# Optimization experiments

Hardware: AMD Instinct MI355X
Metric: run time of the kernel (lower is better)

## Reference

```python
import jax, jax.numpy as jnp
import numpy as np

WS = 8            # current window
PRETRAIN = 8      # pretrain window
HEADS = 8
C = 256
UNITS = C // HEADS
SHIFT = WS // 2   # shift_mode=1 -> shift_dir=[1,1], apply_shift True (H,W > WS)
EPS = 1.55e-5
LOG100 = float(np.log(100.0))

# ---- static relative-position index and log-spaced coord table (SwinV2 CPB) ----
_c = np.arange(WS)
_rel_h = _c[:, None] - _c[None, :] + (WS - 1)          # [WS,WS] in [0, 2WS-2]
REL_INDEX = (_rel_h[:, None, :, None] * (2 * WS - 1) + _rel_h[None, :, None, :]).reshape(WS * WS, WS * WS)
_r = np.arange(-(WS - 1), WS, dtype=np.float32)
_t = np.stack(np.meshgrid(_r, _r, indexing='ij'), axis=-1).reshape(-1, 2)  # [(2WS-1)^2, 2]
_t = _t / (PRETRAIN - 1) * 8.0
CPB_TABLE = np.sign(_t) * np.log2(1.0 + np.abs(_t)) / np.log2(8.0)


def _shift_mask(H, W):
    # region labels per Swin shift mask: segments (dim-WS, WS-SHIFT, SHIFT) for shift_dir=+1
    def seg(n):
        s = np.zeros(n, np.int32)
        s[n - WS:n - SHIFT] = 1
        s[n - SHIFT:] = 2
        return s
    img = seg(H)[:, None] * 3 + seg(W)[None, :] + 1      # [H,W]
    img = img.reshape(H // WS, WS, W // WS, WS).transpose(0, 2, 1, 3).reshape(-1, WS * WS)
    d = img[:, :, None] - img[:, None, :]
    return np.where(d == 0, 0.0, -100.0).astype(np.float32)  # [nW, WS^2, WS^2]

SHIFT_MASK = _shift_mask(256, 256)


def _partition(t, H, W):
    # [B,H,W,C] -> [B,nW,heads,WS^2,units]
    B = t.shape[0]
    t = t.reshape(B, H // WS, WS, W // WS, WS, HEADS, UNITS)
    t = t.transpose(0, 1, 3, 5, 2, 4, 6)
    return t.reshape(B, (H // WS) * (W // WS), HEADS, WS * WS, UNITS)


def _reverse(t, H, W):
    B = t.shape[0]
    t = t.reshape(B, H // WS, W // WS, HEADS, WS, WS, UNITS)
    t = t.transpose(0, 1, 4, 2, 5, 3, 6)
    return t.reshape(B, H, W, C)


def _l2n(t):
    return t / jnp.sqrt(jnp.maximum(jnp.sum(t * t, axis=-1, keepdims=True), EPS))


def setup_inputs():
    key = jax.random.key(0)
    ks = jax.random.split(key, 6)
    return {
        'x': jax.random.normal(ks[0], (2, 256, 256, C), jnp.float32),
        'qkv_w': jax.random.normal(ks[1], (C, 3 * C), jnp.float32) * 0.02,
        'q_bias': jnp.zeros((C,), jnp.float32),
        'v_bias': jnp.zeros((C,), jnp.float32),
        'scale': jnp.full((HEADS, 1, 1), np.log(10.0), jnp.float32),
        'cpb_w1': jax.random.normal(ks[2], (2, 512), jnp.float32) * 0.02,
        'cpb_b1': jnp.zeros((512,), jnp.float32),
        'cpb_w2': jax.random.normal(ks[3], (512, HEADS), jnp.float32) * 0.02,
        'proj_w': jax.random.normal(ks[4], (C, C), jnp.float32) * 0.02,
        'proj_b': jnp.zeros((C,), jnp.float32),
    }


def reference(x, qkv_w, q_bias, v_bias, scale, cpb_w1, cpb_b1, cpb_w2, proj_w, proj_b):
    B, H, W, _ = x.shape
    qkv = x @ qkv_w + jnp.concatenate([q_bias, jnp.zeros_like(q_bias), v_bias])
    qkv = jnp.roll(qkv, (-SHIFT, -SHIFT), axis=(1, 2))
    q, k, v = jnp.split(qkv, 3, axis=-1)
    q = _l2n(_partition(q, H, W))          # [B,nW,h,WS^2,u]
    k = _l2n(_partition(k, H, W))
    v = _partition(v, H, W)
    logit_scale = jnp.exp(jnp.minimum(scale, LOG100))  # [h,1,1]
    attn = jnp.einsum('bwhqd,bwhkd->bwhqk', q * logit_scale, k)
    # continuous relative position bias
    cpb = jax.nn.relu(jnp.asarray(CPB_TABLE) @ cpb_w1 + cpb_b1) @ cpb_w2  # [(2WS-1)^2, h]
    bias = 16.0 * jax.nn.sigmoid(cpb[REL_INDEX])                          # [WS^2,WS^2,h]
    bias = bias.transpose(2, 0, 1)                                        # [h,WS^2,WS^2]
    attn = attn + bias[None, None] + jnp.asarray(SHIFT_MASK)[None, :, None]
    attn = jax.nn.softmax(attn, axis=-1)
    out = jnp.einsum('bwhqk,bwhkd->bwhqd', attn, v)
    out = _reverse(out, H, W)
    out = jnp.roll(out, (SHIFT, SHIFT), axis=(1, 2))
    return out @ proj_w + proj_b
```

## Files before the change

kernel.cpp:

```cpp
#include <hip/hip_runtime.h>


typedef _Float16 f16;
typedef _Float16 f16x4 __attribute__((ext_vector_type(4)));
typedef _Float16 f16x8 __attribute__((ext_vector_type(8)));
typedef float f32x4 __attribute__((ext_vector_type(4)));

#define LOG100 4.6051701859880914f
#define EPS_L2 1.55e-5f

__device__ __forceinline__ int seg2(int p) { return (p >= 248) + (p >= 252); }

__global__ __launch_bounds__(512) void k_prep(
    const float* __restrict__ cpb_w1, const float* __restrict__ cpb_b1,
    const float* __restrict__ cpb_w2, const float* __restrict__ qkv_w,
    const float* __restrict__ proj_w,
    float* __restrict__ biasfrag, f16* __restrict__ w_t, f16* __restrict__ p_t)
{
    int tid = threadIdx.x;
    if (blockIdx.x == 0) {
        __shared__ float Lw1[1024];
        __shared__ float Lb1[512];
        __shared__ float Lw2[4096];
        __shared__ float part[450 * 8];
        __shared__ float cpb[225 * 8];
        #pragma unroll
        for (int i = tid; i < 1024; i += 512) Lw1[i] = cpb_w1[i];
        if (tid < 512) Lb1[tid] = cpb_b1[tid];
        #pragma unroll
        for (int i = tid; i < 4096; i += 512) Lw2[i] = cpb_w2[i];
        __syncthreads();
        {
            int e = tid >> 1, half = tid & 1;
            if (e < 225) {
                int a = e / 15, b2 = e % 15;
                float xa = (float)(a - 7) * (8.0f / 7.0f);
                float xb = (float)(b2 - 7) * (8.0f / 7.0f);
                float t0 = (xa < 0.f ? -1.f : 1.f) * log2f(1.0f + fabsf(xa)) * (1.0f / 3.0f);
                float t1 = (xb < 0.f ? -1.f : 1.f) * log2f(1.0f + fabsf(xb)) * (1.0f / 3.0f);
                float acc[8] = {0.f, 0.f, 0.f, 0.f, 0.f, 0.f, 0.f, 0.f};
                int j0 = half << 8;
                #pragma unroll 4
                for (int j = j0; j < j0 + 256; ++j) {
                    float hh = fmaxf(t0 * Lw1[j] + t1 * Lw1[512 + j] + Lb1[j], 0.0f);
                    #pragma unroll
                    for (int h = 0; h < 8; ++h) acc[h] += hh * Lw2[j * 8 + h];
                }
                #pragma unroll
                for (int h = 0; h < 8; ++h) part[tid * 8 + h] = acc[h];
            }
        }
        __syncthreads();
        if (tid < 225) {
            #pragma unroll
            for (int h = 0; h < 8; ++h)
                cpb[tid * 8 + h] = part[tid * 16 + h] + part[tid * 16 + 8 + h];
        }
        __syncthreads();
        for (int f = tid; f < 32768; f += 512) {
            int r = f & 3, lane = (f >> 2) & 63, nt = (f >> 8) & 3, mt = (f >> 10) & 3, h = (f >> 12) & 7;
            int k = mt * 16 + ((lane >> 4) << 2) + r;
            int q = nt * 16 + (lane & 15);
            int idx = ((q >> 3) - (k >> 3) + 7) * 15 + ((q & 7) - (k & 7) + 7);
            float c = cpb[idx * 8 + h];
            biasfrag[f] = 16.0f / (1.0f + expf(-c));
        }
    } else {
        int base = (blockIdx.x - 1) * 512 + tid;
        const int stride = 128 * 512;
        for (int i = base; i < 768 * 256; i += stride) {
            int n = i >> 8, k = i & 255;
            w_t[i] = (f16)qkv_w[k * 768 + n];
        }
        for (int i = base; i < 256 * 256; i += stride) {
            int n = i >> 8, k = i & 255;
            p_t[i] = (f16)proj_w[k * 256 + n];
        }
    }
}

__global__ __launch_bounds__(512, 3) void k_fused(
    const float* __restrict__ x, const f16* __restrict__ w_t,
    const float* __restrict__ q_bias, const float* __restrict__ v_bias,
    const float* __restrict__ scale, const float* __restrict__ biasfrag,
    const f16* __restrict__ p_t, const float* __restrict__ proj_b,
    float* __restrict__ out)
{
    __shared__ char L[65536];
    const int tid = threadIdx.x;
    const int lane = tid & 63;
    const int h = tid >> 6;
    const int l15 = lane & 15, g = lane >> 4;
    const int bw = blockIdx.x;
    const int win = bw & 1023, b = bw >> 10;
    const int wh = win >> 5, ww = win & 31;
    char* wb = L + 32768 + (h << 12);
    const f32x4 fz = {0.f, 0.f, 0.f, 0.f};
    const bool boundary = (wh == 31) || (ww == 31);

    {
        int pos = tid >> 3, tc = tid & 7;
        int i2 = ((wh << 3) + (pos >> 3) + 4) & 255;
        int j2 = ((ww << 3) + (pos & 7) + 4) & 255;
        const float* xr = x + ((((long)b << 8) + i2) * 256 + j2) * 256;
        int swz = (pos & 7) << 4;
        #pragma unroll
        for (int rep = 0; rep < 4; ++rep) {
            int ch = rep * 64 + tc * 8;
            float4 v0 = *reinterpret_cast<const float4*>(xr + ch);
            float4 v1 = *reinterpret_cast<const float4*>(xr + ch + 4);
            f16x8 hv = { (f16)v0.x, (f16)v0.y, (f16)v0.z, (f16)v0.w,
                         (f16)v1.x, (f16)v1.y, (f16)v1.z, (f16)v1.w };
            *reinterpret_cast<f16x8*>(L + ((pos * 512 + ch * 2) ^ swz)) = hv;
        }
    }
    __syncthreads();

    f16x8 qa[4], kb[4], vf[2][2];

    {
        f32x4 aqk[4][4];
        #pragma unroll
        for (int i = 0; i < 4; ++i)
            #pragma unroll
            for (int j = 0; j < 4; ++j) aqk[i][j] = fz;

        #pragma unroll
        for (int ks = 0; ks < 8; ++ks) {
            f16x8 xf[4], wqk[4];
            #pragma unroll
            for (int mt = 0; mt < 4; ++mt) {
                int row = mt * 16 + l15;
                xf[mt] = *reinterpret_cast<const f16x8*>(
                    L + ((row * 512 + ks * 64 + g * 16) ^ ((row & 7) << 4)));
            }
            #pragma unroll
            for (int ci = 0; ci < 4; ++ci) {
                int p = ci >> 1, ct = ci & 1;
                wqk[ci] = *reinterpret_cast<const f16x8*>(
                    w_t + ((p << 8) + (h << 5) + ct * 16 + l15) * 256 + ks * 32 + g * 8);
            }
            #pragma unroll
            for (int ci = 0; ci < 4; ++ci)
                #pragma unroll
                for (int mt = 0; mt < 4; ++mt)
                    aqk[ci][mt] = __builtin_amdgcn_mfma_f32_16x16x32_f16(wqk[ci], xf[mt], aqk[ci][mt], 0, 0, 0);
        }

        {
            float ls = __expf(fminf(scale[h], LOG100));
            float qb0[4], qb1[4];
            #pragma unroll
            for (int r = 0; r < 4; ++r) {
                qb0[r] = q_bias[(h << 5) + (g << 2) + r];
                qb1[r] = q_bias[(h << 5) + 16 + (g << 2) + r];
            }
            #pragma unroll
            for (int nt = 0; nt < 4; ++nt) {
                int pix = nt * 16 + l15;
                float t0[4], t1[4], s2 = 0.f;
                #pragma unroll
                for (int r = 0; r < 4; ++r) {
                    t0[r] = aqk[0][nt][r] + qb0[r];
                    t1[r] = aqk[1][nt][r] + qb1[r];
                    s2 += t0[r] * t0[r] + t1[r] * t1[r];
                }
                s2 += __shfl_xor(s2, 16); s2 += __shfl_xor(s2, 32);
                float iv = ls / sqrtf(fmaxf(s2, EPS_L2));
                int sw = (pix & 7) << 4;
                f16x4 p0 = { (f16)(t0[0] * iv), (f16)(t0[1] * iv), (f16)(t0[2] * iv), (f16)(t0[3] * iv) };
                f16x4 p1 = { (f16)(t1[0] * iv), (f16)(t1[1] * iv), (f16)(t1[2] * iv), (f16)(t1[3] * iv) };
                *reinterpret_cast<f16x4*>(wb + ((pix * 64 + (g << 3)) ^ sw)) = p0;
                *reinterpret_cast<f16x4*>(wb + ((pix * 64 + 32 + (g << 3)) ^ sw)) = p1;
            }
            #pragma unroll
            for (int nt = 0; nt < 4; ++nt)
                qa[nt] = *reinterpret_cast<const f16x8*>(
                    wb + (((nt * 16 + l15) * 64 + g * 16) ^ ((l15 & 7) << 4)));
        }
        {
            #pragma unroll
            for (int nt = 0; nt < 4; ++nt) {
                int pix = nt * 16 + l15;
                float t0[4], t1[4], s2 = 0.f;
                #pragma unroll
                for (int r = 0; r < 4; ++r) {
                    t0[r] = aqk[2][nt][r];
                    t1[r] = aqk[3][nt][r];
                    s2 += t0[r] * t0[r] + t1[r] * t1[r];
                }
                s2 += __shfl_xor(s2, 16); s2 += __shfl_xor(s2, 32);
                float iv = 1.0f / sqrtf(fmaxf(s2, EPS_L2));
                int sw = (pix & 7) << 4;
                f16x4 p0 = { (f16)(t0[0] * iv), (f16)(t0[1] * iv), (f16)(t0[2] * iv), (f16)(t0[3] * iv) };
                f16x4 p1 = { (f16)(t1[0] * iv), (f16)(t1[1] * iv), (f16)(t1[2] * iv), (f16)(t1[3] * iv) };
                *reinterpret_cast<f16x4*>(wb + ((pix * 64 + (g << 3)) ^ sw)) = p0;
                *reinterpret_cast<f16x4*>(wb + ((pix * 64 + 32 + (g << 3)) ^ sw)) = p1;
            }
            #pragma unroll
            for (int nt = 0; nt < 4; ++nt)
                kb[nt] = *reinterpret_cast<const f16x8*>(
                    wb + (((nt * 16 + l15) * 64 + g * 16) ^ ((l15 & 7) << 4)));
        }
    }

    {
        f32x4 av[4][2];
        #pragma unroll
        for (int mt = 0; mt < 4; ++mt) { av[mt][0] = fz; av[mt][1] = fz; }
        #pragma unroll
        for (int ks = 0; ks < 8; ++ks) {
            f16x8 xf[4], wv[2];
            #pragma unroll
            for (int mt = 0; mt < 4; ++mt) {
                int row = mt * 16 + l15;
                xf[mt] = *reinterpret_cast<const f16x8*>(
                    L + ((row * 512 + ks * 64 + g * 16) ^ ((row & 7) << 4)));
            }
            #pragma unroll
            for (int nt = 0; nt < 2; ++nt)
                wv[nt] = *reinterpret_cast<const f16x8*>(
                    w_t + (512 + (h << 5) + nt * 16 + l15) * 256 + ks * 32 + g * 8);
            #pragma unroll
            for (int mt = 0; mt < 4; ++mt)
                #pragma unroll
                for (int nt = 0; nt < 2; ++nt)
                    av[mt][nt] = __builtin_amdgcn_mfma_f32_16x16x32_f16(xf[mt], wv[nt], av[mt][nt], 0, 0, 0);
        }
        float b0 = v_bias[(h << 5) + l15], b1 = v_bias[(h << 5) + 16 + l15];
        #pragma unroll
        for (int mt = 0; mt < 4; ++mt)
            #pragma unroll
            for (int nt = 0; nt < 2; ++nt) {
                float bsel = nt ? b1 : b0;
                f32x4 avv = av[mt][nt];
                f16x4 pk = { (f16)(avv[0] + bsel), (f16)(avv[1] + bsel),
                             (f16)(avv[2] + bsel), (f16)(avv[3] + bsel) };
                int u = nt * 16 + l15;
                int pix0 = mt * 16 + (g << 2);
                *reinterpret_cast<f16x4*>(wb + ((u * 128 + pix0 * 2) ^ ((u & 7) << 4))) = pk;
            }
        #pragma unroll
        for (int nt = 0; nt < 2; ++nt)
            #pragma unroll
            for (int ks = 0; ks < 2; ++ks)
                vf[nt][ks] = *reinterpret_cast<const f16x8*>(
                    wb + (((nt * 16 + l15) * 128 + ks * 64 + g * 16) ^ ((l15 & 7) << 4)));
    }

    f16x4 oh[4][2];
    #pragma unroll
    for (int c = 0; c < 2; ++c) {
        #pragma unroll
        for (int n2 = 0; n2 < 2; ++n2) {
            const int nt = c * 2 + n2;
            const int qrow = nt * 16 + l15;
            f32x4 st[4];
            #pragma unroll
            for (int mt = 0; mt < 4; ++mt)
                st[mt] = __builtin_amdgcn_mfma_f32_16x16x32_f16(kb[mt], qa[nt], fz, 0, 0, 0);
            #pragma unroll
            for (int mt = 0; mt < 4; ++mt)
                st[mt] += *reinterpret_cast<const f32x4*>(
                    biasfrag + ((((h * 4 + mt) * 4 + nt) * 64 + lane) << 2));
            if (boundary) {
                int lq = seg2((wh << 3) + (qrow >> 3)) * 3 + seg2((ww << 3) + (qrow & 7));
                #pragma unroll
                for (int mt = 0; mt < 4; ++mt)
                    #pragma unroll
                    for (int r = 0; r < 4; ++r) {
                        int k = mt * 16 + (g << 2) + r;
                        int lk = seg2((wh << 3) + (k >> 3)) * 3 + seg2((ww << 3) + (k & 7));
                        if (lq != lk) st[mt][r] -= 100.0f;
                    }
            }
            float mx = st[0][0];
            #pragma unroll
            for (int mt = 0; mt < 4; ++mt)
                #pragma unroll
                for (int r = 0; r < 4; ++r) mx = fmaxf(mx, st[mt][r]);
            mx = fmaxf(mx, __shfl_xor(mx, 16));
            mx = fmaxf(mx, __shfl_xor(mx, 32));
            float sm = 0.f;
            #pragma unroll
            for (int mt = 0; mt < 4; ++mt)
                #pragma unroll
                for (int r = 0; r < 4; ++r) {
                    float e = __expf(st[mt][r] - mx);
                    st[mt][r] = e;
                    sm += e;
                }
            sm += __shfl_xor(sm, 16);
            sm += __shfl_xor(sm, 32);
            float inv = 1.0f / sm;
            int sw = (qrow & 7) << 4;
            int rowb = (qrow & 31) * 128;
            #pragma unroll
            for (int mt = 0; mt < 4; ++mt) {
                f16x4 pk = { (f16)(st[mt][0] * inv), (f16)(st[mt][1] * inv),
                             (f16)(st[mt][2] * inv), (f16)(st[mt][3] * inv) };
                *reinterpret_cast<f16x4*>(wb + ((rowb + mt * 32 + (g << 3)) ^ sw)) = pk;
            }
        }
        #pragma unroll
        for (int m2 = 0; m2 < 2; ++m2) {
            const int mt = c * 2 + m2;
            int row = m2 * 16 + l15;
            int swz = (row & 7) << 4;
            f16x8 pa0 = *reinterpret_cast<const f16x8*>(wb + ((row * 128 + g * 16) ^ swz));
            f16x8 pa1 = *reinterpret_cast<const f16x8*>(wb + ((row * 128 + 64 + g * 16) ^ swz));
            #pragma unroll
            for (int nt = 0; nt < 2; ++nt) {
                f32x4 t = __builtin_amdgcn_mfma_f32_16x16x32_f16(pa0, vf[nt][0], fz, 0, 0, 0);
                t = __builtin_amdgcn_mfma_f32_16x16x32_f16(pa1, vf[nt][1], t, 0, 0, 0);
                oh[mt][nt] = f16x4{ (f16)t[0], (f16)t[1], (f16)t[2], (f16)t[3] };
            }
        }
    }

    __syncthreads();
    #pragma unroll
    for (int mt = 0; mt < 4; ++mt)
        #pragma unroll
        for (int r = 0; r < 4; ++r) {
            int q = mt * 16 + (g << 2) + r;
            #pragma unroll
            for (int nt = 0; nt < 2; ++nt) {
                int ch = (h << 5) + nt * 16 + l15;
                *reinterpret_cast<f16*>(L + ((q * 512 + ch * 2) ^ ((q & 7) << 4))) =
                    oh[mt][nt][r];
            }
        }
    __syncthreads();

    const int c0 = h << 5;
    f32x4 pc[4][2];
    #pragma unroll
    for (int mt = 0; mt < 4; ++mt) { pc[mt][0] = fz; pc[mt][1] = fz; }
    #pragma unroll
    for (int ks = 0; ks < 8; ++ks) {
        f16x8 a[4], bfr[2];
        #pragma unroll
        for (int mt = 0; mt < 4; ++mt) {
            int q = mt * 16 + l15;
            a[mt] = *reinterpret_cast<const f16x8*>(
                L + ((q * 512 + ks * 64 + g * 16) ^ ((q & 7) << 4)));
        }
        #pragma unroll
        for (int nt = 0; nt < 2; ++nt)
            bfr[nt] = *reinterpret_cast<const f16x8*>(
                p_t + (c0 + nt * 16 + l15) * 256 + ks * 32 + g * 8);
        #pragma unroll
        for (int mt = 0; mt < 4; ++mt)
            #pragma unroll
            for (int nt = 0; nt < 2; ++nt)
                pc[mt][nt] = __builtin_amdgcn_mfma_f32_16x16x32_f16(a[mt], bfr[nt], pc[mt][nt], 0, 0, 0);
    }
    float pb0 = proj_b[c0 + l15], pb1 = proj_b[c0 + 16 + l15];
    #pragma unroll
    for (int mt = 0; mt < 4; ++mt)
        #pragma unroll
        for (int r = 0; r < 4; ++r) {
            int q = mt * 16 + (g << 2) + r;
            int i = ((wh << 3) + (q >> 3) + 4) & 255;
            int j = ((ww << 3) + (q & 7) + 4) & 255;
            long addr = (((long)b * 256 + i) * 256 + j) * 256;
            out[addr + c0 + l15]      = pc[mt][0][r] + pb0;
            out[addr + c0 + 16 + l15] = pc[mt][1][r] + pb1;
        }
}

extern "C" void kernel_launch(void* const* d_in, const int* in_sizes, int n_in,
                              void* d_out, int out_size, void* d_ws, size_t ws_size,
                              hipStream_t stream) {
    const float* x      = (const float*)d_in[0];
    const float* qkv_w  = (const float*)d_in[1];
    const float* q_bias = (const float*)d_in[2];
    const float* v_bias = (const float*)d_in[3];
    const float* scale  = (const float*)d_in[4];
    const float* cpb_w1 = (const float*)d_in[5];
    const float* cpb_b1 = (const float*)d_in[6];
    const float* cpb_w2 = (const float*)d_in[7];
    const float* proj_w = (const float*)d_in[8];
    const float* proj_b = (const float*)d_in[9];
    float* out = (float*)d_out;

    char* ws = (char*)d_ws;
    float* biasfrag = (float*)(ws);
    f16* w_t  = (f16*)(ws + 131072);
    f16* p_t  = (f16*)(ws + 524288);

    hipLaunchKernelGGL(k_prep, dim3(129), dim3(512), 0, stream,
                       cpb_w1, cpb_b1, cpb_w2, qkv_w, proj_w, biasfrag, w_t, p_t);
    hipLaunchKernelGGL(k_fused, dim3(2048), dim3(512), 0, stream,
                       x, w_t, q_bias, v_bias, scale, biasfrag, p_t, proj_b, out);
}
```

Baseline: 265.3 us.

## Split Q/K projection into sequential passes to cut registers and raise occupancy

The fused Q and K projection, which held 16 accumulator tiles live at once, is split into two sequential passes of 8 tiles each via a lambda. The launch bound goes from 3 to 4 blocks per SM so the compiler must fit in fewer registers. V staging now writes into the x tile region of shared memory behind an added block barrier, presumably to free space or avoid conflicts. This trades a second pass over the x fragment loads and an extra __syncthreads for higher occupancy, with a risk of register spilling.

Result: no change. 268.9 us (+1.4%).

```diff
diff --git a/kernel.cpp b/kernel.cpp
--- a/kernel.cpp
+++ b/kernel.cpp
@@ -79,7 +79,7 @@
     }
 }
 
-__global__ __launch_bounds__(512, 3) void k_fused(
+__global__ __launch_bounds__(512, 4) void k_fused(
     const float* __restrict__ x, const f16* __restrict__ w_t,
     const float* __restrict__ q_bias, const float* __restrict__ v_bias,
     const float* __restrict__ scale, const float* __restrict__ biasfrag,
@@ -95,6 +95,7 @@
     const int win = bw & 1023, b = bw >> 10;
     const int wh = win >> 5, ww = win & 31;
     char* wb = L + 32768 + (h << 12);
+    char* vtr = L + (h << 12);
     const f32x4 fz = {0.f, 0.f, 0.f, 0.f};
     const bool boundary = (wh == 31) || (ww == 31);
 
@@ -116,18 +117,17 @@
     }
     __syncthreads();
 
-    f16x8 qa[4], kb[4], vf[2][2];
-
-    {
-        f32x4 aqk[4][4];
-        #pragma unroll
-        for (int i = 0; i < 4; ++i)
-            #pragma unroll
-            for (int j = 0; j < 4; ++j) aqk[i][j] = fz;
-
+    f16x8 qa[4], kb[4];
+
+    auto qk_pass = [&](int p, float ls, bool addb, f16x8 frag[4]) {
+        f32x4 acc[2][4];
+        #pragma unroll
+        for (int i = 0; i < 2; ++i)
+            #pragma unroll
+            for (int j = 0; j < 4; ++j) acc[i][j] = fz;
         #pragma unroll
         for (int ks = 0; ks < 8; ++ks) {
-            f16x8 xf[4], wqk[4];
+            f16x8 xf[4], wf[2];
             #pragma unroll
             for (int mt = 0; mt < 4; ++mt) {
                 int row = mt * 16 + l15;
@@ -135,75 +135,49 @@
                     L + ((row * 512 + ks * 64 + g * 16) ^ ((row & 7) << 4)));
             }
             #pragma unroll
-            for (int ci = 0; ci < 4; ++ci) {
-                int p = ci >> 1, ct = ci & 1;
-                wqk[ci] = *reinterpret_cast<const f16x8*>(
+            for (int ct = 0; ct < 2; ++ct)
+                wf[ct] = *reinterpret_cast<const f16x8*>(
                     w_t + ((p << 8) + (h << 5) + ct * 16 + l15) * 256 + ks * 32 + g * 8);
-            }
-            #pragma unroll
-            for (int ci = 0; ci < 4; ++ci)
+            #pragma unroll
+            for (int ct = 0; ct < 2; ++ct)
                 #pragma unroll
                 for (int mt = 0; mt < 4; ++mt)
-                    aqk[ci][mt] = __builtin_amdgcn_mfma_f32_16x16x32_f16(wqk[ci], xf[mt], aqk[ci][mt], 0, 0, 0);
-        }
-
-        {
-            float ls = __expf(fminf(scale[h], LOG100));
-            float qb0[4], qb1[4];
+                    acc[ct][mt] = __builtin_amdgcn_mfma_f32_16x16x32_f16(wf[ct], xf[mt], acc[ct][mt], 0, 0, 0);
+        }
+        float qb0[4], qb1[4];
+        #pragma unroll
+        for (int r = 0; r < 4; ++r) {
+            qb0[r] = addb ? q_bias[(h << 5) + (g << 2) + r] : 0.f;
+            qb1[r] = addb ? q_bias[(h << 5) + 16 + (g << 2) + r] : 0.f;
+        }
+        #pragma unroll
+        for (int nt = 0; nt < 4; ++nt) {
+            int pix = nt * 16 + l15;
+            float t0[4], t1[4], s2 = 0.f;
             #pragma unroll
             for (int r = 0; r < 4; ++r) {
-                qb0[r] = q_bias[(h << 5) + (g << 2) + r];
-                qb1[r] = q_bias[(h << 5) + 16 + (g << 2) + r];
-            }
-            #pragma unroll
-            for (int nt = 0; nt < 4; ++nt) {
-                int pix = nt * 16 + l15;
-                float t0[4], t1[4], s2 = 0.f;
-                #pragma unroll
-                for (int r = 0; r < 4; ++r) {
-                    t0[r] = aqk[0][nt][r] + qb0[r];
-                    t1[r] = aqk[1][nt][r] + qb1[r];
-                    s2 += t0[r] * t0[r] + t1[r] * t1[r];
-                }
-                s2 += __shfl_xor(s2, 16); s2 += __shfl_xor(s2, 32);
-                float iv = ls / sqrtf(fmaxf(s2, EPS_L2));
-                int sw = (pix & 7) << 4;
-                f16x4 p0 = { (f16)(t0[0] * iv), (f16)(t0[1] * iv), (f16)(t0[2] * iv), (f16)(t0[3] * iv) };
-                f16x4 p1 = { (f16)(t1[0] * iv), (f16)(t1[1] * iv), (f16)(t1[2] * iv), (f16)(t1[3] * iv) };
-                *reinterpret_cast<f16x4*>(wb + ((pix * 64 + (g << 3)) ^ sw)) = p0;
-                *reinterpret_cast<f16x4*>(wb + ((pix * 64 + 32 + (g << 3)) ^ sw)) = p1;
-            }
-            #pragma unroll
-            for (int nt = 0; nt < 4; ++nt)
-                qa[nt] = *reinterpret_cast<const f16x8*>(
-                    wb + (((nt * 16 + l15) * 64 + g * 16) ^ ((l15 & 7) << 4)));
-        }
-        {
-            #pragma unroll
-            for (int nt = 0; nt < 4; ++nt) {
-                int pix = nt * 16 + l15;
-                float t0[4], t1[4], s2 = 0.f;
-                #pragma unroll
-                for (int r = 0; r < 4; ++r) {
-                    t0[r] = aqk[2][nt][r];
-                    t1[r] = aqk[3][nt][r];
-                    s2 += t0[r] * t0[r] + t1[r] * t1[r];
-                }
-                s2 += __shfl_xor(s2, 16); s2 += __shfl_xor(s2, 32);
-                float iv = 1.0f / sqrtf(fmaxf(s2, EPS_L2));
-                int sw = (pix & 7) << 4;
-                f16x4 p0 = { (f16)(t0[0] * iv), (f16)(t0[1] * iv), (f16)(t0[2] * iv), (f16)(t0[3] * iv) };
-                f16x4 p1 = { (f16)(t1[0] * iv), (f16)(t1[1] * iv), (f16)(t1[2] * iv), (f16)(t1[3] * iv) };
-                *reinterpret_cast<f16x4*>(wb + ((pix * 64 + (g << 3)) ^ sw)) = p0;
-                *reinterpret_cast<f16x4*>(wb + ((pix * 64 + 32 + (g << 3)) ^ sw)) = p1;
-            }
-            #pragma unroll
-            for (int nt = 0; nt < 4; ++nt)
-                kb[nt] = *reinterpret_cast<const f16x8*>(
-                    wb + (((nt * 16 + l15) * 64 + g * 16) ^ ((l15 & 7) << 4)));
-        }
-    }
-
+                t0[r] = acc[0][nt][r] + qb0[r];
+                t1[r] = acc[1][nt][r] + qb1[r];
+                s2 += t0[r] * t0[r] + t1[r] * t1[r];
+            }
+            s2 += __shfl_xor(s2, 16); s2 += __shfl_xor(s2, 32);
+            float iv = ls / sqrtf(fmaxf(s2, EPS_L2));
+            int sw = (pix & 7) << 4;
+            f16x4 p0 = { (f16)(t0[0] * iv), (f16)(t0[1] * iv), (f16)(t0[2] * iv), (f16)(t0[3] * iv) };
+            f16x4 p1 = { (f16)(t1[0] * iv), (f16)(t1[1] * iv), (f16)(t1[2] * iv), (f16)(t1[3] * iv) };
+            *reinterpret_cast<f16x4*>(wb + ((pix * 64 + (g << 3)) ^ sw)) = p0;
+            *reinterpret_cast<f16x4*>(wb + ((pix * 64 + 32 + (g << 3)) ^ sw)) = p1;
+        }
+        #pragma unroll
+        for (int nt = 0; nt < 4; ++nt)
+            frag[nt] = *reinterpret_cast<const f16x8*>(
+                wb + (((nt * 16 + l15) * 64 + g * 16) ^ ((l15 & 7) << 4)));
+    };
+
+    qk_pass(0, __expf(fminf(scale[h], LOG100)), true, qa);
+    qk_pass(1, 1.0f, false, kb);
+
+    f16x8 vf[2][2];
     {
         f32x4 av[4][2];
         #pragma unroll
@@ -227,6 +201,7 @@
                 for (int nt = 0; nt < 2; ++nt)
                     av[mt][nt] = __builtin_amdgcn_mfma_f32_16x16x32_f16(xf[mt], wv[nt], av[mt][nt], 0, 0, 0);
         }
+        __syncthreads();
         float b0 = v_bias[(h << 5) + l15], b1 = v_bias[(h << 5) + 16 + l15];
         #pragma unroll
         for (int mt = 0; mt < 4; ++mt)
@@ -238,14 +213,14 @@
                              (f16)(avv[2] + bsel), (f16)(avv[3] + bsel) };
                 int u = nt * 16 + l15;
                 int pix0 = mt * 16 + (g << 2);
-                *reinterpret_cast<f16x4*>(wb + ((u * 128 + pix0 * 2) ^ ((u & 7) << 4))) = pk;
+                *reinterpret_cast<f16x4*>(vtr + ((u * 128 + pix0 * 2) ^ ((u & 7) << 4))) = pk;
             }
         #pragma unroll
         for (int nt = 0; nt < 2; ++nt)
             #pragma unroll
             for (int ks = 0; ks < 2; ++ks)
                 vf[nt][ks] = *reinterpret_cast<const f16x8*>(
-                    wb + (((nt * 16 + l15) * 128 + ks * 64 + g * 16) ^ ((l15 & 7) << 4)));
+                    vtr + (((nt * 16 + l15) * 128 + ks * 64 + g * 16) ^ ((l15 & 7) << 4)));
     }
 
     f16x4 oh[4][2];
```
